# Kernel tuning notes

Hardware: AMD Instinct MI355X
Metric: run time of the kernel (lower is better)

Reference implementation:

```python
import jax, jax.numpy as jnp
import numpy as np

B, T, H, NSPK = 8, 1024, 1024, 2
LN_EPS = 1e-5


def setup_inputs() -> dict:
    key = jax.random.key(0)
    ks = jax.random.split(key, 12)
    s = 1.0 / np.sqrt(H)
    return {
        "x": jax.random.normal(ks[0], (B, T, H), jnp.float32),
        "qmask": jax.random.uniform(ks[1], (B, T, NSPK), jnp.float32),
        "dia_len": jax.random.randint(ks[2], (B,), T // 2, T + 1),
        "wp": 8,
        "wf": 8,
        "W_msg": jax.random.normal(ks[3], (H, H), jnp.float32) * s,
        "b_msg": jax.random.normal(ks[4], (H,), jnp.float32) * s,
        "W_self": jax.random.normal(ks[5], (H, H), jnp.float32) * s,
        "b_self": jax.random.normal(ks[6], (H,), jnp.float32) * s,
        "W_out": jax.random.normal(ks[7], (H, H), jnp.float32) * s,
        "b_out": jax.random.normal(ks[8], (H,), jnp.float32) * s,
        "gamma": jnp.ones((H,), jnp.float32),
        "beta": jnp.zeros((H,), jnp.float32),
    }


def reference(x, qmask, dia_len, wp, wf, W_msg, b_msg, W_self, b_self, W_out, b_out, gamma, beta):
    Bb, Tt, Hh = x.shape
    spk = jnp.argmax(qmask, axis=-1)                     # [B,T]
    pos = jnp.arange(Tt)
    offs = jnp.arange(-wp, wf + 1)                       # [W]
    idx = pos[:, None] + offs[None, :]                   # [T,W] window indices
    vlen = dia_len[:, None, None]                        # [B,1,1]
    valid = (idx[None] >= 0) & (idx[None] <= vlen - 1)   # [B,T,W]
    idxc = jnp.clip(idx, 0, Tt - 1)
    nb = jnp.take(x, idxc, axis=1)                       # [B,T,W,H]
    nb_spk = jnp.take(spk, idxc, axis=1)                 # [B,T,W]
    same = (nb_spk == spk[:, :, None]).astype(x.dtype)
    w = jnp.where(valid, 0.5 + 0.5 * same, 0.0)          # speaker weights, masked
    cnt = jnp.maximum(valid.sum(-1).astype(x.dtype), 1.0)  # window sizes [B,T]
    msg = jnp.einsum('btw,btwh->bth', w, nb) / cnt[..., None]
    h = x @ W_self + b_self + msg @ W_msg + b_msg        # per-node fusion
    node_valid = (pos[None, :] < dia_len[:, None])[..., None]
    out = jnp.where(node_valid, h, x)                    # nodes past dia_len keep x
    y = jax.nn.relu(out) @ W_out + b_out                 # dropout = identity (eval)
    z = x + y
    mean = z.mean(-1, keepdims=True)
    var = z.var(-1, keepdims=True)
    return gamma * (z - mean) / jnp.sqrt(var + LN_EPS) + beta
```

## Files before the change

kernel.cpp:

```cpp
#include <hip/hip_runtime.h>


typedef unsigned short u16;
typedef float floatx4 __attribute__((ext_vector_type(4)));
typedef short shortx8 __attribute__((ext_vector_type(8)));

#define T_ 1024
#define H_ 1024

__device__ __forceinline__ float bf2f(u16 v) {
    return __uint_as_float(((unsigned)v) << 16);
}
__device__ __forceinline__ u16 f2bf(float f) {
    unsigned u = __float_as_uint(f);
    return (u16)((u + 0x7fffu + ((u >> 16) & 1u)) >> 16);
}
__device__ __forceinline__ void async16(const void* g, void* l) {
    __builtin_amdgcn_global_load_lds(
        (__attribute__((address_space(1))) void*)g,
        (__attribute__((address_space(3))) void*)l, 16, 0, 0);
}
__device__ __forceinline__ void barrier_mem() {
    asm volatile("" ::: "memory");
    __builtin_amdgcn_s_barrier();
    asm volatile("" ::: "memory");
}

__global__ __launch_bounds__(256)
void transpose_pack(const float* __restrict__ Wself, const float* __restrict__ Wmsg,
                    const float* __restrict__ Wout,
                    u16* __restrict__ wt_cat, u16* __restrict__ wt_out)
{
    __shared__ float s[32][33];
    const int wid = blockIdx.z;
    const float* src = (wid == 0) ? Wself : ((wid == 1) ? Wmsg : Wout);
    const int n0 = blockIdx.x * 32, k0 = blockIdx.y * 32;
    const int tx = threadIdx.x & 31, ty = threadIdx.x >> 5;
#pragma unroll
    for (int i = 0; i < 4; ++i) {
        int k = k0 + ty + 8 * i;
        s[ty + 8 * i][tx] = src[(size_t)k * H_ + n0 + tx];
    }
    __syncthreads();
#pragma unroll
    for (int i = 0; i < 4; ++i) {
        int n = n0 + ty + 8 * i;
        u16 v = f2bf(s[tx][ty + 8 * i]);
        if (wid < 2) wt_cat[(size_t)n * 2048 + wid * 1024 + k0 + tx] = v;
        else         wt_out[(size_t)n * 1024 + k0 + tx] = v;
    }
}

__global__ __launch_bounds__(256)
void msg_pack(const float* __restrict__ x, const float* __restrict__ qmask,
              const int* __restrict__ dia_len, u16* __restrict__ xcat)
{
    __shared__ u16 sx[32][1024];
    const int tid = threadIdx.x;
    const int b = blockIdx.y;
    const int t0 = blockIdx.x * 16;
    const int dlen = dia_len[b];
    const int c4 = tid * 4;
    const float* xb = x + (size_t)b * T_ * H_;

    unsigned spkmask = 0;
#pragma unroll 4
    for (int r = 0; r < 32; ++r) {
        int row = t0 - 8 + r;
        row = row < 0 ? 0 : (row > T_ - 1 ? T_ - 1 : row);
        const float* q = qmask + ((size_t)b * T_ + row) * 2;
        spkmask |= (q[1] > q[0] ? 1u : 0u) << r;
        float4 v = *(const float4*)(xb + (size_t)row * H_ + c4);
        ushort4 u;
        u.x = f2bf(v.x); u.y = f2bf(v.y); u.z = f2bf(v.z); u.w = f2bf(v.w);
        *(ushort4*)&sx[r][c4] = u;
    }
    __syncthreads();

    for (int lt = 0; lt < 16; ++lt) {
        const int t = t0 + lt;
        const unsigned cs = (spkmask >> (lt + 8)) & 1u;
        float a0 = 0.f, a1 = 0.f, a2 = 0.f, a3 = 0.f;
        int cnt = 0;
#pragma unroll
        for (int o = 0; o < 17; ++o) {
            const int idx = t + o - 8;
            if (idx >= 0 && idx < dlen) {
                const float w = (((spkmask >> (lt + o)) & 1u) == cs) ? 1.0f : 0.5f;
                ++cnt;
                ushort4 u = *(const ushort4*)&sx[lt + o][c4];
                a0 += w * bf2f(u.x); a1 += w * bf2f(u.y);
                a2 += w * bf2f(u.z); a3 += w * bf2f(u.w);
            }
        }
        const float inv = 1.0f / (float)(cnt > 0 ? cnt : 1);
        ushort4 m;
        m.x = f2bf(a0 * inv); m.y = f2bf(a1 * inv);
        m.z = f2bf(a2 * inv); m.w = f2bf(a3 * inv);
        const size_t rowg = (size_t)b * T_ + t;
        *(ushort4*)&xcat[rowg * 2048 + 1024 + c4] = m;
        *(ushort4*)&xcat[rowg * 2048 + c4] = *(const ushort4*)&sx[lt + 8][c4];
    }
}

template <int K, int EPI>
__global__ __launch_bounds__(256, 2)
void gemm_bt(const u16* __restrict__ A, const u16* __restrict__ Bt,
             const float* __restrict__ bias1, const float* __restrict__ bias2,
             const float* __restrict__ X, const int* __restrict__ dia_len,
             u16* __restrict__ Rout, float* __restrict__ Zout)
{
    constexpr int NT = K / 64;
    static_assert(NT >= 2, "need >=2 K-tiles");
    __shared__ u16 sA[2][128 * 64];
    __shared__ u16 sB[2][128 * 64];
    const int tid = threadIdx.x;

    const int bid = blockIdx.x;
    const int xcd = bid & 7, li = bid >> 3;
    const int mt = xcd * 8 + (li >> 3);
    const int nt = li & 7;
    const int bm = mt * 128, bn = nt * 128;

    const int wave = tid >> 6, lane = tid & 63;
    const int wr = wave >> 1, wc = wave & 1;
    const int lrow = lane & 15, lq = lane >> 4;

    const int srow = tid >> 3;
    const int sl   = (tid & 7) ^ (srow & 7);
    const u16* Asrc = A + (size_t)(bm + srow) * K + sl * 8;
    const u16* Bsrc = Bt + (size_t)(bn + srow) * K + sl * 8;

    auto stage = [&](int t, int buf) {
        const int k0 = t * 64;
#pragma unroll
        for (int q = 0; q < 4; ++q)
            async16(Asrc + (size_t)q * 32 * K + k0, &sA[buf][q * 2048 + tid * 8]);
#pragma unroll
        for (int q = 0; q < 4; ++q)
            async16(Bsrc + (size_t)q * 32 * K + k0, &sB[buf][q * 2048 + tid * 8]);
    };

    floatx4 acc[4][4];
#pragma unroll
    for (int i = 0; i < 4; ++i)
#pragma unroll
        for (int j = 0; j < 4; ++j)
            acc[i][j] = (floatx4){0.f, 0.f, 0.f, 0.f};

    const int xk = lrow & 7;
    const int paBase = (wr * 64 + lrow) * 64;
    const int pbBase = (wc * 64 + lrow) * 64;
    const int s0 = (lq ^ xk) * 8;
    const int s1 = ((4 + lq) ^ xk) * 8;

    stage(0, 0);
    stage(1, 1);
    asm volatile("s_waitcnt vmcnt(8)" ::: "memory");
    barrier_mem();

    for (int t = 0; t < NT; ++t) {
        if (t >= 1 && t + 1 < NT) stage(t + 1, (t + 1) & 1);

        const u16* curA = &sA[t & 1][0];
        const u16* curB = &sB[t & 1][0];
        shortx8 a0[4], b0[4], a1[4], b1[4];
#pragma unroll
        for (int j = 0; j < 4; ++j)
            b0[j] = *(const shortx8*)(curB + pbBase + j * 1024 + s0);
#pragma unroll
        for (int i = 0; i < 4; ++i)
            a0[i] = *(const shortx8*)(curA + paBase + i * 1024 + s0);
#pragma unroll
        for (int j = 0; j < 4; ++j)
            b1[j] = *(const shortx8*)(curB + pbBase + j * 1024 + s1);
#pragma unroll
        for (int i = 0; i < 4; ++i)
            a1[i] = *(const shortx8*)(curA + paBase + i * 1024 + s1);

        __builtin_amdgcn_s_setprio(1);
#pragma unroll
        for (int i = 0; i < 4; ++i)
#pragma unroll
            for (int j = 0; j < 4; ++j)
                acc[i][j] = __builtin_amdgcn_mfma_f32_16x16x32_bf16(
                    a0[i], b0[j], acc[i][j], 0, 0, 0);
#pragma unroll
        for (int i = 0; i < 4; ++i)
#pragma unroll
            for (int j = 0; j < 4; ++j)
                acc[i][j] = __builtin_amdgcn_mfma_f32_16x16x32_bf16(
                    a1[i], b1[j], acc[i][j], 0, 0, 0);
        __builtin_amdgcn_s_setprio(0);

        if (t + 1 < NT) {
            asm volatile("s_waitcnt vmcnt(0)" ::: "memory");
            barrier_mem();
        }
    }

    const int dl = (EPI == 1) ? dia_len[bm >> 10] : 0;
#pragma unroll
    for (int i = 0; i < 4; ++i) {
        const int row0 = bm + wr * 64 + i * 16 + lq * 4;
#pragma unroll
        for (int j = 0; j < 4; ++j) {
            const int col = bn + wc * 64 + j * 16 + lrow;
#pragma unroll
            for (int r = 0; r < 4; ++r) {
                const int row = row0 + r;
                const float v = acc[i][j][r];
                if (EPI == 1) {
                    const float h = v + bias1[col] + bias2[col];
                    float outv;
                    if ((row & (T_ - 1)) < dl) {
                        outv = h;
                    } else {
                        outv = X[(size_t)row * H_ + col];
                    }
                    Rout[(size_t)row * H_ + col] = f2bf(fmaxf(outv, 0.f));
                } else {
                    const float z = X[(size_t)row * H_ + col] + v + bias1[col];
                    Zout[(size_t)row * H_ + col] = z;
                }
            }
        }
    }
}

__global__ __launch_bounds__(256)
void ln_kernel(const float* __restrict__ Z, const float* __restrict__ gamma,
               const float* __restrict__ beta, float* __restrict__ out)
{
    const int row = blockIdx.x;
    const int tid = threadIdx.x;
    const size_t base = (size_t)row * H_ + tid * 4;
    float4 v = *(const float4*)(Z + base);
    float s = v.x + v.y + v.z + v.w;
    float q = v.x * v.x + v.y * v.y + v.z * v.z + v.w * v.w;
#pragma unroll
    for (int off = 32; off > 0; off >>= 1) {
        s += __shfl_down(s, off);
        q += __shfl_down(q, off);
    }
    __shared__ float ps[4], pq[4];
    const int wave = tid >> 6, lane = tid & 63;
    if (lane == 0) { ps[wave] = s; pq[wave] = q; }
    __syncthreads();
    const float S = ps[0] + ps[1] + ps[2] + ps[3];
    const float Q = pq[0] + pq[1] + pq[2] + pq[3];
    const float mean = S * (1.0f / 1024.0f);
    const float var = Q * (1.0f / 1024.0f) - mean * mean;
    const float inv = rsqrtf(var + 1e-5f);
    float4 g = *(const float4*)(gamma + tid * 4);
    float4 bt = *(const float4*)(beta + tid * 4);
    float4 o;
    o.x = g.x * (v.x - mean) * inv + bt.x;
    o.y = g.y * (v.y - mean) * inv + bt.y;
    o.z = g.z * (v.z - mean) * inv + bt.z;
    o.w = g.w * (v.w - mean) * inv + bt.w;
    *(float4*)(out + base) = o;
}

extern "C" void kernel_launch(void* const* d_in, const int* in_sizes, int n_in,
                              void* d_out, int out_size, void* d_ws, size_t ws_size,
                              hipStream_t stream)
{
    (void)in_sizes; (void)n_in; (void)out_size; (void)ws_size;
    const float* x       = (const float*)d_in[0];
    const float* qmask   = (const float*)d_in[1];
    const int*   dia_len = (const int*)d_in[2];
    const float* W_msg   = (const float*)d_in[5];
    const float* b_msg   = (const float*)d_in[6];
    const float* W_self  = (const float*)d_in[7];
    const float* b_self  = (const float*)d_in[8];
    const float* W_out   = (const float*)d_in[9];
    const float* b_out   = (const float*)d_in[10];
    const float* gamma   = (const float*)d_in[11];
    const float* beta    = (const float*)d_in[12];
    float* out = (float*)d_out;

    char* ws = (char*)d_ws;
    u16*   xcat   = (u16*)ws;
    u16*   rbuf   = (u16*)(ws + (size_t)(32u << 20));
    u16*   wt_cat = (u16*)(ws + (size_t)(48u << 20));
    u16*   wt_out = (u16*)(ws + (size_t)(52u << 20));
    float* zbuf   = (float*)ws;

    transpose_pack<<<dim3(32, 32, 3), 256, 0, stream>>>(W_self, W_msg, W_out, wt_cat, wt_out);
    msg_pack<<<dim3(64, 8), 256, 0, stream>>>(x, qmask, dia_len, xcat);
    gemm_bt<2048, 1><<<dim3(512), 256, 0, stream>>>(xcat, wt_cat, b_self, b_msg,
                                                    x, dia_len, rbuf, nullptr);
    gemm_bt<1024, 2><<<dim3(512), 256, 0, stream>>>(rbuf, wt_out, b_out, nullptr,
                                                    x, nullptr, nullptr, zbuf);
    ln_kernel<<<dim3(8192), 256, 0, stream>>>(zbuf, gamma, beta, out);
}
```

Before: 223.1 us.

## Fuse weight transpose with message pack and move GEMMs to 8-wave blocks

Merges the weight transpose/bf16 pack kernel and the message-pack kernel into one launch, dispatched by block index, which removes a kernel launch. The two GEMM kernels now use 512 threads per block. Each of the 8 waves computes a 32x64 sub-tile instead of 64x64, and each thread issues half as many async loads per stage. The intent is more waves to hide latency. The costs are a lower MFMA-to-LDS-read ratio per wave and a tight register budget from launch_bounds(512,4), which could cause spills, while LDS use still caps how many blocks fit per CU.

Result: faster. 206.4 us (-7.5%).

```diff
diff --git a/kernel.cpp b/kernel.cpp
--- a/kernel.cpp
+++ b/kernel.cpp
@@ -27,38 +27,43 @@
 }
 
 __global__ __launch_bounds__(256)
-void transpose_pack(const float* __restrict__ Wself, const float* __restrict__ Wmsg,
-                    const float* __restrict__ Wout,
-                    u16* __restrict__ wt_cat, u16* __restrict__ wt_out)
-{
-    __shared__ float s[32][33];
-    const int wid = blockIdx.z;
-    const float* src = (wid == 0) ? Wself : ((wid == 1) ? Wmsg : Wout);
-    const int n0 = blockIdx.x * 32, k0 = blockIdx.y * 32;
-    const int tx = threadIdx.x & 31, ty = threadIdx.x >> 5;
-#pragma unroll
-    for (int i = 0; i < 4; ++i) {
-        int k = k0 + ty + 8 * i;
-        s[ty + 8 * i][tx] = src[(size_t)k * H_ + n0 + tx];
-    }
-    __syncthreads();
-#pragma unroll
-    for (int i = 0; i < 4; ++i) {
-        int n = n0 + ty + 8 * i;
-        u16 v = f2bf(s[tx][ty + 8 * i]);
-        if (wid < 2) wt_cat[(size_t)n * 2048 + wid * 1024 + k0 + tx] = v;
-        else         wt_out[(size_t)n * 1024 + k0 + tx] = v;
-    }
-}
-
-__global__ __launch_bounds__(256)
-void msg_pack(const float* __restrict__ x, const float* __restrict__ qmask,
-              const int* __restrict__ dia_len, u16* __restrict__ xcat)
+void prep_kernel(const float* __restrict__ x, const float* __restrict__ qmask,
+                 const int* __restrict__ dia_len,
+                 const float* __restrict__ Wself, const float* __restrict__ Wmsg,
+                 const float* __restrict__ Wout,
+                 u16* __restrict__ xcat, u16* __restrict__ wt_cat,
+                 u16* __restrict__ wt_out)
 {
     __shared__ u16 sx[32][1024];
     const int tid = threadIdx.x;
-    const int b = blockIdx.y;
-    const int t0 = blockIdx.x * 16;
+    const int bx = blockIdx.x;
+
+    if (bx >= 512) {
+        const int id = bx - 512;
+        const int wid = id >> 10;
+        const int rest = id & 1023;
+        const int n0 = (rest & 31) * 32, k0 = (rest >> 5) * 32;
+        const float* src = (wid == 0) ? Wself : ((wid == 1) ? Wmsg : Wout);
+        float (*s)[33] = reinterpret_cast<float (*)[33]>(&sx[0][0]);
+        const int tx = tid & 31, ty = tid >> 5;
+#pragma unroll
+        for (int i = 0; i < 4; ++i) {
+            int k = k0 + ty + 8 * i;
+            s[ty + 8 * i][tx] = src[(size_t)k * H_ + n0 + tx];
+        }
+        __syncthreads();
+#pragma unroll
+        for (int i = 0; i < 4; ++i) {
+            int n = n0 + ty + 8 * i;
+            u16 v = f2bf(s[tx][ty + 8 * i]);
+            if (wid < 2) wt_cat[(size_t)n * 2048 + wid * 1024 + k0 + tx] = v;
+            else         wt_out[(size_t)n * 1024 + k0 + tx] = v;
+        }
+        return;
+    }
+
+    const int b = bx >> 6;
+    const int t0 = (bx & 63) * 16;
     const int dlen = dia_len[b];
     const int c4 = tid * 4;
     const float* xb = x + (size_t)b * T_ * H_;
@@ -104,7 +109,7 @@
 }
 
 template <int K, int EPI>
-__global__ __launch_bounds__(256, 2)
+__global__ __launch_bounds__(512, 4)
 void gemm_bt(const u16* __restrict__ A, const u16* __restrict__ Bt,
              const float* __restrict__ bias1, const float* __restrict__ bias2,
              const float* __restrict__ X, const int* __restrict__ dia_len,
@@ -133,30 +138,28 @@
 
     auto stage = [&](int t, int buf) {
         const int k0 = t * 64;
-#pragma unroll
-        for (int q = 0; q < 4; ++q)
-            async16(Asrc + (size_t)q * 32 * K + k0, &sA[buf][q * 2048 + tid * 8]);
-#pragma unroll
-        for (int q = 0; q < 4; ++q)
-            async16(Bsrc + (size_t)q * 32 * K + k0, &sB[buf][q * 2048 + tid * 8]);
+        async16(Asrc + k0,                    &sA[buf][tid * 8]);
+        async16(Asrc + (size_t)64 * K + k0,   &sA[buf][4096 + tid * 8]);
+        async16(Bsrc + k0,                    &sB[buf][tid * 8]);
+        async16(Bsrc + (size_t)64 * K + k0,   &sB[buf][4096 + tid * 8]);
     };
 
-    floatx4 acc[4][4];
-#pragma unroll
-    for (int i = 0; i < 4; ++i)
+    floatx4 acc[2][4];
+#pragma unroll
+    for (int i = 0; i < 2; ++i)
 #pragma unroll
         for (int j = 0; j < 4; ++j)
             acc[i][j] = (floatx4){0.f, 0.f, 0.f, 0.f};
 
     const int xk = lrow & 7;
-    const int paBase = (wr * 64 + lrow) * 64;
+    const int paBase = (wr * 32 + lrow) * 64;
     const int pbBase = (wc * 64 + lrow) * 64;
     const int s0 = (lq ^ xk) * 8;
     const int s1 = ((4 + lq) ^ xk) * 8;
 
     stage(0, 0);
     stage(1, 1);
-    asm volatile("s_waitcnt vmcnt(8)" ::: "memory");
+    asm volatile("s_waitcnt vmcnt(4)" ::: "memory");
     barrier_mem();
 
     for (int t = 0; t < NT; ++t) {
@@ -164,29 +167,29 @@
 
         const u16* curA = &sA[t & 1][0];
         const u16* curB = &sB[t & 1][0];
-        shortx8 a0[4], b0[4], a1[4], b1[4];
+        shortx8 a0[2], a1[2], b0[4], b1[4];
 #pragma unroll
         for (int j = 0; j < 4; ++j)
             b0[j] = *(const shortx8*)(curB + pbBase + j * 1024 + s0);
 #pragma unroll
-        for (int i = 0; i < 4; ++i)
+        for (int i = 0; i < 2; ++i)
             a0[i] = *(const shortx8*)(curA + paBase + i * 1024 + s0);
 #pragma unroll
         for (int j = 0; j < 4; ++j)
             b1[j] = *(const shortx8*)(curB + pbBase + j * 1024 + s1);
 #pragma unroll
-        for (int i = 0; i < 4; ++i)
+        for (int i = 0; i < 2; ++i)
             a1[i] = *(const shortx8*)(curA + paBase + i * 1024 + s1);
 
         __builtin_amdgcn_s_setprio(1);
 #pragma unroll
-        for (int i = 0; i < 4; ++i)
+        for (int i = 0; i < 2; ++i)
 #pragma unroll
             for (int j = 0; j < 4; ++j)
                 acc[i][j] = __builtin_amdgcn_mfma_f32_16x16x32_bf16(
                     a0[i], b0[j], acc[i][j], 0, 0, 0);
 #pragma unroll
-        for (int i = 0; i < 4; ++i)
+        for (int i = 0; i < 2; ++i)
 #pragma unroll
             for (int j = 0; j < 4; ++j)
                 acc[i][j] = __builtin_amdgcn_mfma_f32_16x16x32_bf16(
@@ -201,8 +204,8 @@
 
     const int dl = (EPI == 1) ? dia_len[bm >> 10] : 0;
 #pragma unroll
-    for (int i = 0; i < 4; ++i) {
-        const int row0 = bm + wr * 64 + i * 16 + lq * 4;
+    for (int i = 0; i < 2; ++i) {
+        const int row0 = bm + wr * 32 + i * 16 + lq * 4;
 #pragma unroll
         for (int j = 0; j < 4; ++j) {
             const int col = bn + wc * 64 + j * 16 + lrow;
@@ -287,11 +290,12 @@
     u16*   wt_out = (u16*)(ws + (size_t)(52u << 20));
     float* zbuf   = (float*)ws;
 
-    transpose_pack<<<dim3(32, 32, 3), 256, 0, stream>>>(W_self, W_msg, W_out, wt_cat, wt_out);
-    msg_pack<<<dim3(64, 8), 256, 0, stream>>>(x, qmask, dia_len, xcat);
-    gemm_bt<2048, 1><<<dim3(512), 256, 0, stream>>>(xcat, wt_cat, b_self, b_msg,
+    prep_kernel<<<dim3(3584), 256, 0, stream>>>(x, qmask, dia_len,
+                                                W_self, W_msg, W_out,
+                                                xcat, wt_cat, wt_out);
+    gemm_bt<2048, 1><<<dim3(512), 512, 0, stream>>>(xcat, wt_cat, b_self, b_msg,
                                                     x, dia_len, rbuf, nullptr);
-    gemm_bt<1024, 2><<<dim3(512), 256, 0, stream>>>(rbuf, wt_out, b_out, nullptr,
+    gemm_bt<1024, 2><<<dim3(512), 512, 0, stream>>>(rbuf, wt_out, b_out, nullptr,
                                                     x, nullptr, nullptr, zbuf);
     ln_kernel<<<dim3(8192), 256, 0, stream>>>(zbuf, gamma, beta, out);
 }
```
